# Kernel optimization log

Measured on AMD Instinct MI355X. Metric: run time of the kernel, lower is better.

## Reference

```python
import math
import jax, jax.numpy as jnp
import numpy as np

EPS = 1e-7
MAX_TANH_ARG = 1.0 - 1e-5

def _norm(x):
    return jnp.sqrt(jnp.sum(x * x, axis=-1, keepdims=True)).clip(EPS)

def logmap0(x):  # Poincare ball, c=1
    n = _norm(x)
    return jnp.arctanh(jnp.clip(n, EPS, MAX_TANH_ARG)) * x / n

def expmap0(v):
    n = _norm(v)
    return jnp.tanh(n) * v / n

def mobius_add(x, y):
    x2 = jnp.sum(x * x, -1, keepdims=True)
    y2 = jnp.sum(y * y, -1, keepdims=True)
    xy = jnp.sum(x * y, -1, keepdims=True)
    num = (1 + 2 * xy + y2) * x + (1 - x2) * y
    den = (1 + 2 * xy + x2 * y2).clip(EPS)
    return num / den

def plin(x, w, b):  # PoincareLinear: tangent-space affine map
    return expmap0(logmap0(x) @ w + b)

def layer_norm(x, eps=1e-6):  # elementwise_affine=False
    m = x.mean(-1, keepdims=True)
    v = ((x - m) ** 2).mean(-1, keepdims=True)
    return (x - m) / jnp.sqrt(v + eps)

def _beta(a, b):
    return math.exp(math.lgamma(a) + math.lgamma(b) - math.lgamma(a + b))

D, H, FF = 1024, 16, 4096
HD = D // H
BETA_N = _beta(D / 2, 0.5)   # beta(n/2, 1/2) for full dim
BETA_H = _beta(HD / 2, 0.5)  # beta(ni/2, 1/2) for head dim


def setup_inputs() -> dict:
    key = jax.random.key(0)
    ks = jax.random.split(key, 20)
    B, S = 4, 1024
    x = expmap0(0.02 * jax.random.normal(ks[0], (B, S, D), jnp.float32))
    t_emb = jax.random.normal(ks[1], (B, 1, D), jnp.float32)
    g = lambda k, sh: 0.02 * jax.random.normal(k, sh, jnp.float32)
    return {
        'x': x, 't_emb': t_emb,
        'w_q': g(ks[2], (D, D)), 'b_q': jnp.zeros((D,), jnp.float32),
        'w_k': g(ks[3], (D, D)), 'b_k': jnp.zeros((D,), jnp.float32),
        'w_v': g(ks[4], (D, D)), 'b_v': jnp.zeros((D,), jnp.float32),
        'w_o': g(ks[5], (D, D)), 'b_o': jnp.zeros((D,), jnp.float32),
        'w_f1': g(ks[6], (D, FF)), 'b_f1': jnp.zeros((FF,), jnp.float32),
        'w_f2': g(ks[7], (FF, D)), 'b_f2': jnp.zeros((D,), jnp.float32),
        'w_ada': g(ks[8], (D, 6 * D)), 'b_ada': jnp.zeros((6 * D,), jnp.float32),
    }


def _to_heads(p):
    # beta-split: logmap0, split per head, scale by beta_ni/beta_n, expmap0
    B, S, _ = p.shape
    t = logmap0(p).reshape(B, S, H, HD) * (BETA_H / BETA_N)
    return expmap0(jnp.transpose(t, (0, 2, 1, 3)))  # [B,H,S,HD]


def _from_heads(ph):
    # beta-concat: logmap0 per head, scale by beta_n/beta_ni, concat, expmap0
    B, _, S, _ = ph.shape
    t = logmap0(ph) * (BETA_N / BETA_H)
    t = jnp.transpose(t, (0, 2, 1, 3)).reshape(B, S, D)
    return expmap0(t)


def reference(x, t_emb, w_q, b_q, w_k, b_k, w_v, b_v, w_o, b_o,
              w_f1, b_f1, w_f2, b_f2, w_ada, b_ada):
    ada = t_emb @ w_ada + b_ada  # [B,1,6D]
    sh_msa, sc_msa, g_msa, sh_mlp, sc_mlp, g_mlp = jnp.split(ada, 6, axis=-1)

    # --- attention block ---
    residual = x
    xn = layer_norm(logmap0(x))
    xm = expmap0(xn * (1 + sc_msa) + sh_msa)

    q = _to_heads(plin(xm, w_q, b_q))
    k = _to_heads(plin(xm, w_k, b_k))
    v = _to_heads(plin(xm, w_v, b_v))

    qt, kt, vt = logmap0(q), logmap0(k), logmap0(v)
    scores = jnp.einsum('bhqd,bhkd->bhqk', qt, kt) / math.sqrt(HD)
    attn = jax.nn.softmax(scores, axis=-1)
    out_h = expmap0(jnp.einsum('bhqk,bhkd->bhqd', attn, vt))  # [B,H,S,HD]

    attn_out = plin(_from_heads(out_h), w_o, b_o)
    attn_t = g_msa * logmap0(attn_out)
    x = mobius_add(residual, expmap0(attn_t))

    # --- FFN block ---
    residual = x
    xn = layer_norm(logmap0(x))
    xm = expmap0(xn * (1 + sc_mlp) + sh_mlp)
    ff = plin(plin(xm, w_f1, b_f1), w_f2, b_f2)
    ff_t = g_mlp * logmap0(ff)
    return mobius_add(residual, expmap0(ff_t))
```

## Files before the change

### kernel.cpp

```cpp
#include <hip/hip_runtime.h>
#include <cmath>


constexpr int kD  = 1024;
constexpr int kH  = 16;
constexpr int kHD = 64;
constexpr int kFF = 4096;
constexpr int kB  = 4;
constexpr int kS  = 1024;
constexpr int kN  = kB * kS;

#define EPSF 1e-7f
#define MTAF (1.0f - 1e-5f)
#define LOG2E 1.4426950408889634f

typedef unsigned int uint32;
typedef unsigned short ushort16;
typedef __attribute__((ext_vector_type(8))) short short8x;
typedef __attribute__((ext_vector_type(4))) float floatx4;

__device__ __forceinline__ ushort16 f2b(float f) {
  union { float f; uint32 u; } x; x.f = f;
  uint32 r = x.u + 0x7fffu + ((x.u >> 16) & 1u);
  return (ushort16)(r >> 16);
}
__device__ __forceinline__ float b2f(ushort16 u) {
  union { uint32 u; float f; } x; x.u = ((uint32)u) << 16;
  return x.f;
}
__device__ __forceinline__ void load_b4(const ushort16* p, float v[4]) {
  uint2 u = *(const uint2*)p;
  v[0] = b2f((ushort16)(u.x & 0xffff)); v[1] = b2f((ushort16)(u.x >> 16));
  v[2] = b2f((ushort16)(u.y & 0xffff)); v[3] = b2f((ushort16)(u.y >> 16));
}
__device__ __forceinline__ void store_b4(ushort16* p, const float v[4]) {
  uint2 u;
  u.x = (uint32)f2b(v[0]) | ((uint32)f2b(v[1]) << 16);
  u.y = (uint32)f2b(v[2]) | ((uint32)f2b(v[3]) << 16);
  *(uint2*)p = u;
}

__device__ __forceinline__ float atanh_clipped(float n) {
  float c = fminf(n, MTAF);
  return 0.5f * logf((1.0f + c) / (1.0f - c));
}
__device__ __forceinline__ float logmap0_scale(float nraw) {
  float n = fmaxf(nraw, EPSF);
  return atanh_clipped(n) / n;
}
__device__ __forceinline__ float expmap0_scale(float nraw) {
  float n = fmaxf(nraw, EPSF);
  return tanhf(n) / n;
}
__device__ __forceinline__ float roundtrip_scale(float nraw) {
  float nu = fmaxf(nraw, EPSF);
  float se = tanhf(nu) / nu;
  float nb = fmaxf(se * nraw, EPSF);
  float sl = atanh_clipped(nb) / nb;
  return sl * se;
}

__device__ __forceinline__ float blockReduceSum256(float v, float* s4) {
#pragma unroll
  for (int o = 32; o > 0; o >>= 1) v += __shfl_xor(v, o);
  int wave = threadIdx.x >> 6;
  if ((threadIdx.x & 63) == 0) s4[wave] = v;
  __syncthreads();
  float r = s4[0] + s4[1] + s4[2] + s4[3];
  __syncthreads();
  return r;
}
__device__ __forceinline__ float redSum16(float v) {
#pragma unroll
  for (int o = 8; o > 0; o >>= 1) v += __shfl_xor(v, o);
  return v;
}

__device__ __forceinline__ void async16(const void* g, void* l) {
  __builtin_amdgcn_global_load_lds(
      (const __attribute__((address_space(1))) uint32*)g,
      (__attribute__((address_space(3))) uint32*)l, 16, 0, 0);
}

__device__ __forceinline__ void transpose_tile(const float* __restrict__ src,
                                               ushort16* __restrict__ dst,
                                               int K, int N, int n0, int k0) {
  __shared__ float T[64][65];
  int tid = threadIdx.x;
#pragma unroll
  for (int p = 0; p < 4; ++p) {
    int idx = p * 1024 + tid * 4;
    int r = idx >> 6, c = idx & 63;
    float4 t = *(const float4*)&src[(size_t)(k0 + r) * N + n0 + c];
    T[r][c] = t.x; T[r][c + 1] = t.y; T[r][c + 2] = t.z; T[r][c + 3] = t.w;
  }
  __syncthreads();
#pragma unroll
  for (int p = 0; p < 4; ++p) {
    int idx = p * 1024 + tid * 4;
    int r = idx >> 6, c = idx & 63;
    float v[4] = {T[c][r], T[c + 1][r], T[c + 2][r], T[c + 3][r]};
    store_b4(&dst[(size_t)(n0 + r) * K + k0 + c], v);
  }
}
__global__ __launch_bounds__(256) void k_transpose_bf16(const float* __restrict__ src,
                                                        ushort16* __restrict__ dst,
                                                        int K, int N) {
  transpose_tile(src, dst, K, N, blockIdx.x * 64, blockIdx.y * 64);
}
__global__ __launch_bounds__(256) void k_transpose4(
    const float* __restrict__ s0, const float* __restrict__ s1,
    const float* __restrict__ s2, const float* __restrict__ s3,
    ushort16* __restrict__ d0, ushort16* __restrict__ d1,
    ushort16* __restrict__ d2, ushort16* __restrict__ d3) {
  const float* src = (blockIdx.z == 0) ? s0 : (blockIdx.z == 1) ? s1
                    : (blockIdx.z == 2) ? s2 : s3;
  ushort16* dst = (blockIdx.z == 0) ? d0 : (blockIdx.z == 1) ? d1
                 : (blockIdx.z == 2) ? d2 : d3;
  transpose_tile(src, dst, kD, kD, blockIdx.x * 64, blockIdx.y * 64);
}

__global__ __launch_bounds__(256) void k_ada(const float* __restrict__ t_emb,
                                             const float* __restrict__ w_ada,
                                             const float* __restrict__ b_ada,
                                             float* __restrict__ ada) {
  __shared__ float te[kD];
  __shared__ float part[4][64];
  int b = blockIdx.y;
  int tid = threadIdx.x;
  {
    float4 t = *(const float4*)&t_emb[b * kD + tid * 4];
    te[tid * 4] = t.x; te[tid * 4 + 1] = t.y; te[tid * 4 + 2] = t.z; te[tid * 4 + 3] = t.w;
  }
  __syncthreads();
  int c = tid & 63, kc = tid >> 6;
  int col = blockIdx.x * 64 + c;
  float acc = 0.f;
#pragma unroll 8
  for (int k = kc * 256; k < kc * 256 + 256; ++k)
    acc += te[k] * w_ada[(size_t)k * (6 * kD) + col];
  part[kc][c] = acc;
  __syncthreads();
  if (tid < 64)
    ada[b * 6 * kD + blockIdx.x * 64 + tid] =
        part[0][tid] + part[1][tid] + part[2][tid] + part[3][tid] +
        b_ada[blockIdx.x * 64 + tid];
}

__global__ __launch_bounds__(256) void k_prenorm(const float* __restrict__ x,
                                                 const float* __restrict__ ada,
                                                 int sh_off, int sc_off,
                                                 ushort16* __restrict__ out) {
  __shared__ float sred[4];
  int tok = blockIdx.x;
  int b = tok >> 10;
  int d4 = threadIdx.x * 4;
  float xv[4];
  *(float4*)xv = *(const float4*)&x[(size_t)tok * kD + d4];
  float ss = xv[0] * xv[0] + xv[1] * xv[1] + xv[2] * xv[2] + xv[3] * xv[3];
  ss = blockReduceSum256(ss, sred);
  float sl = logmap0_scale(sqrtf(ss));
  float sum = 0.f;
#pragma unroll
  for (int i = 0; i < 4; ++i) { xv[i] *= sl; sum += xv[i]; }
  sum = blockReduceSum256(sum, sred);
  float mean = sum * (1.0f / kD);
  float vs = 0.f;
#pragma unroll
  for (int i = 0; i < 4; ++i) { xv[i] -= mean; vs += xv[i] * xv[i]; }
  vs = blockReduceSum256(vs, sred);
  float inv = rsqrtf(vs * (1.0f / kD) + 1e-6f);
  float shv[4], scv[4];
  *(float4*)shv = *(const float4*)&ada[b * 6 * kD + sh_off + d4];
  *(float4*)scv = *(const float4*)&ada[b * 6 * kD + sc_off + d4];
  float uu = 0.f;
#pragma unroll
  for (int i = 0; i < 4; ++i) {
    float u = xv[i] * inv * (1.0f + scv[i]) + shv[i];
    xv[i] = u;
    uu += u * u;
  }
  uu = blockReduceSum256(uu, sred);
  float s = roundtrip_scale(sqrtf(uu));
#pragma unroll
  for (int i = 0; i < 4; ++i) xv[i] *= s;
  store_b4(out + (size_t)tok * kD + d4, xv);
}

template <int OUT_BF16, int KSPLIT>
__global__ __launch_bounds__(256) void k_gemm_bf16(
    const ushort16* __restrict__ A,
    const ushort16* __restrict__ Bt0, const ushort16* __restrict__ Bt1,
    const ushort16* __restrict__ Bt2,
    const float* __restrict__ bias0, const float* __restrict__ bias1,
    const float* __restrict__ bias2,
    const float* __restrict__ rowscale,
    void* __restrict__ C0, void* __restrict__ C1, void* __restrict__ C2,
    int M, int N, int K) {
  const ushort16* Bt;
  const float* bias;
  void* C;
  int k_lo, k_hi;
  bool add_bias;
  if (KSPLIT == 1) {
    Bt = (blockIdx.z == 0) ? Bt0 : ((blockIdx.z == 1) ? Bt1 : Bt2);
    bias = (blockIdx.z == 0) ? bias0 : ((blockIdx.z == 1) ? bias1 : bias2);
    C = (blockIdx.z == 0) ? C0 : ((blockIdx.z == 1) ? C1 : C2);
    k_lo = 0; k_hi = K; add_bias = true;
  } else {
    Bt = Bt0; bias = bias0;
    C = (blockIdx.z == 0) ? C0 : C1;
    int kchunk = K / KSPLIT;
    k_lo = blockIdx.z * kchunk; k_hi = k_lo + kchunk;
    add_bias = (blockIdx.z == 0);
  }

  __shared__ __align__(16) ushort16 As[128 * 32];
  __shared__ __align__(16) ushort16 Bs[128 * 32];

  int tid = threadIdx.x;
  int lane = tid & 63;
  int wave = tid >> 6;
  int wm = (wave >> 1) * 64, wn = (wave & 1) * 64;
  int row0 = blockIdx.x * 128, col0 = blockIdx.y * 128;

  int e0 = tid * 8;
  int ar0 = e0 >> 5;
  int ac0 = ((((e0 >> 3) & 3) ^ ((ar0 >> 1) & 3)) << 3);
  int e1 = e0 + 2048;
  int ar1 = e1 >> 5;
  int ac1 = ((((e1 >> 3) & 3) ^ ((ar1 >> 1) & 3)) << 3);
  const ushort16* Ag = A + (size_t)row0 * K;
  const ushort16* Bg = Bt + (size_t)col0 * K;

  int c16 = lane & 15, quad = lane >> 4;
  int sw = (lane >> 1) & 3;
  int cbp = ((quad ^ sw) << 3);

  floatx4 acc[4][4];
#pragma unroll
  for (int i = 0; i < 4; ++i)
#pragma unroll
    for (int j = 0; j < 4; ++j) acc[i][j] = (floatx4)0.f;

  for (int k0 = k_lo; k0 < k_hi; k0 += 32) {
    async16(Ag + (size_t)ar0 * K + k0 + ac0, As + e0);
    async16(Ag + (size_t)ar1 * K + k0 + ac1, As + e1);
    async16(Bg + (size_t)ar0 * K + k0 + ac0, Bs + e0);
    async16(Bg + (size_t)ar1 * K + k0 + ac1, Bs + e1);
    __syncthreads();

    short8x a[4], b[4];
#pragma unroll
    for (int i = 0; i < 4; ++i) {
      a[i] = *(const short8x*)&As[(wm + i * 16 + c16) * 32 + cbp];
      b[i] = *(const short8x*)&Bs[(wn + i * 16 + c16) * 32 + cbp];
    }
#pragma unroll
    for (int i = 0; i < 4; ++i)
#pragma unroll
      for (int j = 0; j < 4; ++j)
        acc[i][j] = __builtin_amdgcn_mfma_f32_16x16x32_bf16(a[i], b[j], acc[i][j], 0, 0, 0);
    __syncthreads();
  }

  float bv[4];
#pragma unroll
  for (int j = 0; j < 4; ++j)
    bv[j] = add_bias ? bias[col0 + wn + j * 16 + c16] : 0.f;
  int rowq = quad * 4;
#pragma unroll
  for (int i = 0; i < 4; ++i) {
    int rbase = row0 + wm + i * 16 + rowq;
    float rs4[4];
#pragma unroll
    for (int r = 0; r < 4; ++r) rs4[r] = rowscale ? rowscale[rbase + r] : 1.0f;
#pragma unroll
    for (int j = 0; j < 4; ++j) {
      int c = col0 + wn + j * 16 + c16;
#pragma unroll
      for (int r = 0; r < 4; ++r) {
        float v = acc[i][j][r] * rs4[r] + bv[j];
        if (KSPLIT == 2) {
          if (blockIdx.z == 0) ((float*)C)[(size_t)(rbase + r) * N + c] = v;
          else ((ushort16*)C)[(size_t)(rbase + r) * N + c] = f2b(v);
        } else if (OUT_BF16) {
          ((ushort16*)C)[(size_t)(rbase + r) * N + c] = f2b(v);
        } else {
          ((float*)C)[(size_t)(rbase + r) * N + c] = v;
        }
      }
    }
  }
}

__global__ __launch_bounds__(256) void k_headsplit_b(const ushort16* __restrict__ q_in,
                                                     ushort16* __restrict__ k_io,
                                                     ushort16* __restrict__ v_io,
                                                     ushort16* __restrict__ qb_out,
                                                     float ratio) {
  __shared__ float sred[4];
  int tok = blockIdx.x;
  int tid = threadIdx.x;
  int d4 = tid * 4;
#pragma unroll
  for (int t = 0; t < 3; ++t) {
    const ushort16* p = (t == 0 ? q_in : (t == 1 ? (const ushort16*)k_io
                                                 : (const ushort16*)v_io)) +
                        (size_t)tok * kD + d4;
    float val[4];
    load_b4(p, val);
    float psq = val[0] * val[0] + val[1] * val[1] + val[2] * val[2] + val[3] * val[3];
    float hsq = redSum16(psq);
    float tot = blockReduceSum256(psq, sred);
    float s1 = roundtrip_scale(sqrtf(tot));
    float c = s1 * ratio;
    float s2 = roundtrip_scale(c * sqrtf(hsq));
    float f = c * s2 * (t == 0 ? (0.125f * LOG2E) : 1.0f);
#pragma unroll
    for (int i = 0; i < 4; ++i) val[i] *= f;
    ushort16* op = (t == 0 ? qb_out : (t == 1 ? k_io : v_io)) + (size_t)tok * kD + d4;
    store_b4(op, val);
    __syncthreads();
  }
}

__global__ __launch_bounds__(256) void k_vtrans_b(const ushort16* __restrict__ v,
                                                  ushort16* __restrict__ vT) {
  __shared__ ushort16 T[64][68];
  int bh = blockIdx.y, b = bh >> 4, h = bh & 15;
  int s0 = blockIdx.x * 64;
  int tid = threadIdx.x;
#pragma unroll
  for (int p = 0; p < 4; ++p) {
    int idx = p * 1024 + tid * 4;
    int r = idx >> 6, d = idx & 63;
    *(uint2*)&T[r][d] = *(const uint2*)&v[(size_t)(b * kS + s0 + r) * kD + h * kHD + d];
  }
  __syncthreads();
#pragma unroll
  for (int p = 0; p < 16; ++p) {
    int idx = p * 256 + tid;
    int d = idx >> 6, c = idx & 63;
    int cp = (c & 32) | ((c & 15) << 1) | ((c >> 4) & 1);
    vT[((size_t)bh * kHD + d) * kS + s0 + cp] = T[c][d];
  }
}

__global__ __launch_bounds__(256) void k_attn_mfma(ushort16* __restrict__ qb,
                                                   const ushort16* __restrict__ kb,
                                                   const ushort16* __restrict__ vT,
                                                   float ratio2) {
  __shared__ __align__(16) ushort16 Ks[2 * 128 * 32];
  __shared__ __align__(16) ushort16 Vs[4 * 64 * 32];
  __shared__ __align__(16) ushort16 Ps[4 * 4 * 16 * 40];
  int bh = blockIdx.x, b = bh >> 4, h = bh & 15;
  int q0 = blockIdx.y * 128;
  int tid = threadIdx.x, lane = tid & 63, wave = tid >> 6;
  int c16 = lane & 15, quad = lane >> 4;
  int sw = (lane >> 1) & 3;
  int cbp = ((quad ^ sw) << 3);
  int wq = wave * 32;

  short8x a_q[2][2];
#pragma unroll
  for (int i = 0; i < 2; ++i)
#pragma unroll
    for (int kk = 0; kk < 2; ++kk)
      a_q[i][kk] = *(const short8x*)&qb[(size_t)(b * kS + q0 + wq + i * 16 + c16) * kD +
                                        h * kHD + kk * 32 + quad * 8];

  short8x ones;
#pragma unroll
  for (int j = 0; j < 8; ++j) ones[j] = (short)0x3F80;

  floatx4 o[2][4], ol[2];
#pragma unroll
  for (int i = 0; i < 2; ++i) {
    ol[i] = (floatx4)0.f;
#pragma unroll
    for (int n = 0; n < 4; ++n) o[i][n] = (floatx4)0.f;
  }

  const ushort16* kbase = kb + ((size_t)b * kS) * kD + h * kHD;
  const ushort16* vbase = vT + (size_t)bh * kHD * kS;

  for (int k0 = 0; k0 < kS; k0 += 128) {
#pragma unroll
    for (int t = 0; t < 2; ++t)
#pragma unroll
      for (int cb2 = 0; cb2 < 2; ++cb2) {
        int e = cb2 * 2048 + tid * 8;
        int key = e >> 5;
        int col = ((((e >> 3) & 3) ^ ((key >> 1) & 3)) << 3);
        async16(kbase + (size_t)(k0 + key) * kD + t * 32 + col, Ks + t * 4096 + e);
      }
#pragma unroll
    for (int t = 0; t < 4; ++t) {
      int e = tid * 8;
      int dd = e >> 5;
      int col = ((((e >> 3) & 3) ^ ((dd >> 1) & 3)) << 3);
      async16(vbase + (size_t)dd * kS + k0 + t * 32 + col, Vs + t * 2048 + e);
    }
    __syncthreads();

#pragma unroll
    for (int i = 0; i < 2; ++i) {
      floatx4 s[8];
#pragma unroll
      for (int n = 0; n < 8; ++n) s[n] = (floatx4)0.f;
#pragma unroll
      for (int kkd = 0; kkd < 2; ++kkd)
#pragma unroll
        for (int n = 0; n < 8; ++n) {
          short8x bk = *(const short8x*)&Ks[kkd * 4096 + (n * 16 + c16) * 32 + cbp];
          s[n] = __builtin_amdgcn_mfma_f32_16x16x32_bf16(a_q[i][kkd], bk, s[n], 0, 0, 0);
        }

#pragma unroll
      for (int r = 0; r < 4; ++r) {
#pragma unroll
        for (int j = 0; j < 4; ++j) {
          uint32 u0 = (uint32)f2b(exp2f(s[2 * j][r]));
          uint32 u1 = (uint32)f2b(exp2f(s[2 * j + 1][r]));
          *(uint32*)&Ps[(((wave * 4 + j) * 16) + (quad * 4 + r)) * 40 + c16 * 2] =
              u0 | (u1 << 16);
        }
      }

#pragma unroll
      for (int kk = 0; kk < 4; ++kk) {
        short8x ap = *(const short8x*)&Ps[(((wave * 4 + kk) * 16) + c16) * 40 + quad * 8];
#pragma unroll
        for (int n = 0; n < 4; ++n) {
          short8x bv = *(const short8x*)&Vs[kk * 2048 + (n * 16 + c16) * 32 + cbp];
          o[i][n] = __builtin_amdgcn_mfma_f32_16x16x32_bf16(ap, bv, o[i][n], 0, 0, 0);
        }
        ol[i] = __builtin_amdgcn_mfma_f32_16x16x32_bf16(ap, ones, ol[i], 0, 0, 0);
      }
    }
    __syncthreads();
  }

#pragma unroll
  for (int i = 0; i < 2; ++i)
#pragma unroll
    for (int r = 0; r < 4; ++r) {
      float invl = 1.0f / ol[i][r];
      float w[4];
      float pssq = 0.f;
#pragma unroll
      for (int n = 0; n < 4; ++n) { w[n] = o[i][n][r] * invl; pssq += w[n] * w[n]; }
      float ssq = redSum16(pssq);
      float coef = roundtrip_scale(sqrtf(ssq)) * ratio2;
      int row = b * kS + q0 + wq + i * 16 + quad * 4 + r;
#pragma unroll
      for (int n = 0; n < 4; ++n)
        qb[(size_t)row * kD + h * kHD + n * 16 + c16] = f2b(coef * w[n]);
    }
}

template <int WIDTH>
__global__ __launch_bounds__(256) void k_rowscale(const ushort16* __restrict__ p,
                                                  float* __restrict__ s) {
  __shared__ float sred[4];
  constexpr int PER = WIDTH / 1024;
  size_t base = (size_t)blockIdx.x * WIDTH;
  float ss = 0.f;
#pragma unroll
  for (int i = 0; i < PER; ++i) {
    float v[4];
    load_b4(p + base + i * 1024 + threadIdx.x * 4, v);
    ss += v[0] * v[0] + v[1] * v[1] + v[2] * v[2] + v[3] * v[3];
  }
  ss = blockReduceSum256(ss, sred);
  if (threadIdx.x == 0) s[blockIdx.x] = roundtrip_scale(sqrtf(ss));
}

__device__ __forceinline__ void mobius_body(float xv[4], float tv[4],
                                            const float* gp, int d4,
                                            float* sred, float outv[4]) {
  float ss = tv[0] * tv[0] + tv[1] * tv[1] + tv[2] * tv[2] + tv[3] * tv[3];
  ss = blockReduceSum256(ss, sred);
  float s5 = roundtrip_scale(sqrtf(ss));
  float gv[4];
  *(float4*)gv = *(const float4*)&gp[d4];
  float at2 = 0.f;
#pragma unroll
  for (int i = 0; i < 4; ++i) {
    float a = gv[i] * s5 * tv[i];
    tv[i] = a;
    at2 += a * a;
  }
  at2 = blockReduceSum256(at2, sred);
  float nyraw = sqrtf(at2);
  float sy = expmap0_scale(nyraw);
  float ynorm = sy * nyraw;
  float y2 = ynorm * ynorm;
  float x2p = 0.f, xyp = 0.f;
#pragma unroll
  for (int i = 0; i < 4; ++i) {
    float y = sy * tv[i];
    tv[i] = y;
    x2p += xv[i] * xv[i];
    xyp += xv[i] * y;
  }
  float x2 = blockReduceSum256(x2p, sred);
  float xy = blockReduceSum256(xyp, sred);
  float cx = 1.0f + 2.0f * xy + y2;
  float cy = 1.0f - x2;
  float den = fmaxf(1.0f + 2.0f * xy + x2 * y2, EPSF);
  float invden = 1.0f / den;
#pragma unroll
  for (int i = 0; i < 4; ++i) outv[i] = (cx * xv[i] + cy * tv[i]) * invden;
}

__global__ __launch_bounds__(256) void k_epilogue2(const float* __restrict__ xres,
                                                   const float* __restrict__ ot0,
                                                   const ushort16* __restrict__ ot1b,
                                                   const float* __restrict__ ada,
                                                   int g_off,
                                                   float* __restrict__ out) {
  __shared__ float sred[4];
  int tok = blockIdx.x;
  int b = tok >> 10;
  size_t base = (size_t)tok * kD;
  int d4 = threadIdx.x * 4;
  float xv[4], tv[4], t1[4];
  *(float4*)tv = *(const float4*)&ot0[base + d4];
  load_b4(ot1b + base + d4, t1);
  *(float4*)xv = *(const float4*)&xres[base + d4];
#pragma unroll
  for (int i = 0; i < 4; ++i) tv[i] += t1[i];
  float outv[4];
  mobius_body(xv, tv, ada + b * 6 * kD + g_off, d4, sred, outv);
  *(float4*)&out[base + d4] = *(float4*)outv;
}

__global__ __launch_bounds__(256) void k_epi_pre(const float* __restrict__ xres,
                                                 const float* __restrict__ ot0,
                                                 const ushort16* __restrict__ ot1b,
                                                 const float* __restrict__ ada,
                                                 float* __restrict__ xmid_out,
                                                 ushort16* __restrict__ lx2_out) {
  __shared__ float sred[4];
  int tok = blockIdx.x;
  int b = tok >> 10;
  size_t base = (size_t)tok * kD;
  int d4 = threadIdx.x * 4;
  float xv[4], tv[4], t1[4];
  *(float4*)tv = *(const float4*)&ot0[base + d4];
  load_b4(ot1b + base + d4, t1);
  *(float4*)xv = *(const float4*)&xres[base + d4];
#pragma unroll
  for (int i = 0; i < 4; ++i) tv[i] += t1[i];
  float xm[4];
  mobius_body(xv, tv, ada + b * 6 * kD + 2 * kD, d4, sred, xm);
  *(float4*)&xmid_out[base + d4] = *(float4*)xm;

  float ss = xm[0] * xm[0] + xm[1] * xm[1] + xm[2] * xm[2] + xm[3] * xm[3];
  ss = blockReduceSum256(ss, sred);
  float sl = logmap0_scale(sqrtf(ss));
  float sum = 0.f;
#pragma unroll
  for (int i = 0; i < 4; ++i) { xm[i] *= sl; sum += xm[i]; }
  sum = blockReduceSum256(sum, sred);
  float mean = sum * (1.0f / kD);
  float vs = 0.f;
#pragma unroll
  for (int i = 0; i < 4; ++i) { xm[i] -= mean; vs += xm[i] * xm[i]; }
  vs = blockReduceSum256(vs, sred);
  float inv = rsqrtf(vs * (1.0f / kD) + 1e-6f);
  float shv[4], scv[4];
  *(float4*)shv = *(const float4*)&ada[b * 6 * kD + 3 * kD + d4];
  *(float4*)scv = *(const float4*)&ada[b * 6 * kD + 4 * kD + d4];
  float uu = 0.f;
#pragma unroll
  for (int i = 0; i < 4; ++i) {
    float u = xm[i] * inv * (1.0f + scv[i]) + shv[i];
    xm[i] = u;
    uu += u * u;
  }
  uu = blockReduceSum256(uu, sred);
  float s = roundtrip_scale(sqrtf(uu));
#pragma unroll
  for (int i = 0; i < 4; ++i) xm[i] *= s;
  store_b4(lx2_out + base + d4, xm);
}

extern "C" void kernel_launch(void* const* d_in, const int* in_sizes, int n_in,
                              void* d_out, int out_size, void* d_ws, size_t ws_size,
                              hipStream_t stream) {
  const float* x     = (const float*)d_in[0];
  const float* t_emb = (const float*)d_in[1];
  const float* w_q = (const float*)d_in[2];  const float* b_q = (const float*)d_in[3];
  const float* w_k = (const float*)d_in[4];  const float* b_k = (const float*)d_in[5];
  const float* w_v = (const float*)d_in[6];  const float* b_v = (const float*)d_in[7];
  const float* w_o = (const float*)d_in[8];  const float* b_o = (const float*)d_in[9];
  const float* w_f1 = (const float*)d_in[10]; const float* b_f1 = (const float*)d_in[11];
  const float* w_f2 = (const float*)d_in[12]; const float* b_f2 = (const float*)d_in[13];
  const float* w_ada = (const float*)d_in[14]; const float* b_ada = (const float*)d_in[15];
  float* out = (float*)d_out;

  constexpr size_t ND = (size_t)kN * kD;
  constexpr size_t NF = (size_t)kN * kFF;
  constexpr size_t DD = (size_t)kD * kD;

  float* ws   = (float*)d_ws;
  float* ada  = ws;
  float* qt   = ada + 6 * kD * kB;
  float* kt   = qt + ND;
  float* vt   = kt + ND;
  ushort16* qbA = (ushort16*)(vt + ND);
  ushort16* kb  = qbA + ND;
  ushort16* vTb = kb + ND;
  ushort16* actB = vTb + ND;
  ushort16* wqT  = actB + NF;
  ushort16* wkT  = wqT + DD;
  ushort16* wvT  = wkT + DD;
  ushort16* woT  = wvT + DD;
  ushort16* wf1T = woT + DD;
  ushort16* wf2T = wf1T + (size_t)kD * kFF;

  double bn = exp(lgamma(512.0) + lgamma(0.5) - lgamma(512.5));
  double bh = exp(lgamma(32.0) + lgamma(0.5) - lgamma(32.5));
  float R1 = (float)(bh / bn);
  float R2 = (float)(bn / bh);

  k_transpose4<<<dim3(16, 16, 4), 256, 0, stream>>>(w_q, w_k, w_v, w_o,
                                                    wqT, wkT, wvT, woT);
  k_transpose_bf16<<<dim3(64, 16), 256, 0, stream>>>(w_f1, wf1T, kD, kFF);
  k_transpose_bf16<<<dim3(16, 64), 256, 0, stream>>>(w_f2, wf2T, kFF, kD);
  k_ada<<<dim3(6 * kD / 64, kB), 256, 0, stream>>>(t_emb, w_ada, b_ada, ada);
  k_prenorm<<<kN, 256, 0, stream>>>(x, ada, 0 * kD, 1 * kD, qbA);
  k_gemm_bf16<1, 1><<<dim3(kN / 128, kD / 128, 3), 256, 0, stream>>>(
      qbA, wqT, wkT, wvT, b_q, b_k, b_v, nullptr, kb, vTb, actB, kN, kD, kD);
  k_headsplit_b<<<kN, 256, 0, stream>>>(kb, vTb, actB, qbA, R1);
  k_vtrans_b<<<dim3(kS / 64, kB * kH), 256, 0, stream>>>(actB, kb);
  k_attn_mfma<<<dim3(kB * kH, kS / 128), 256, 0, stream>>>(qbA, vTb, kb, R2);
  k_rowscale<kD><<<kN, 256, 0, stream>>>(qbA, kt);
  k_gemm_bf16<0, 2><<<dim3(kN / 128, kD / 128, 2), 256, 0, stream>>>(
      qbA, woT, woT, woT, b_o, b_o, b_o, kt, qt, kb, nullptr, kN, kD, kD);
  k_epi_pre<<<kN, 256, 0, stream>>>(x, qt, kb, ada, vt, qbA);
  k_gemm_bf16<1, 1><<<dim3(kN / 128, kFF / 128, 1), 256, 0, stream>>>(
      qbA, wf1T, wf1T, wf1T, b_f1, b_f1, b_f1, nullptr, actB, actB, actB, kN, kFF, kD);
  k_rowscale<kFF><<<kN, 256, 0, stream>>>(actB, kt);
  k_gemm_bf16<0, 2><<<dim3(kN / 128, kD / 128, 2), 256, 0, stream>>>(
      actB, wf2T, wf2T, wf2T, b_f2, b_f2, b_f2, kt, qt, kb, nullptr, kN, kD, kFF);
  k_epilogue2<<<kN, 256, 0, stream>>>(vt, qt, kb, ada, 5 * kD, out);

  (void)in_sizes; (void)n_in; (void)out_size; (void)ws_size;
}
```

Before: 452.2 us.

## Double-buffer GEMM with 256x128 tiles, BK=64, and async prefetch pipeline

Rewrites the bf16 GEMM to use 512-thread blocks over 256x128 output tiles with a K-step of 64. Shared memory is double-buffered, and the loads for step t+2 are issued while the MFMAs for step t run. The waits use explicit vmcnt/lgkmcnt counts and s_setprio around the MFMA bursts. The goal is to hide global-load latency and halve the barriers per K, at the cost of 96KB of LDS per block and a more fragile hand-counted wait scheme.

Result: faster. 432.5 us (-4.4%).

```diff
diff --git a/kernel.cpp b/kernel.cpp
--- a/kernel.cpp
+++ b/kernel.cpp
@@ -188,7 +188,7 @@
 }
 
 template <int OUT_BF16, int KSPLIT>
-__global__ __launch_bounds__(256) void k_gemm_bf16(
+__global__ __launch_bounds__(512, 2) void k_gemm_bf16(
     const ushort16* __restrict__ A,
     const ushort16* __restrict__ Bt0, const ushort16* __restrict__ Bt1,
     const ushort16* __restrict__ Bt2,
@@ -215,27 +215,39 @@
     add_bias = (blockIdx.z == 0);
   }
 
-  __shared__ __align__(16) ushort16 As[128 * 32];
-  __shared__ __align__(16) ushort16 Bs[128 * 32];
+  __shared__ __align__(16) ushort16 As[2 * 256 * 64];
+  __shared__ __align__(16) ushort16 Bs[2 * 128 * 64];
 
   int tid = threadIdx.x;
   int lane = tid & 63;
   int wave = tid >> 6;
-  int wm = (wave >> 1) * 64, wn = (wave & 1) * 64;
-  int row0 = blockIdx.x * 128, col0 = blockIdx.y * 128;
-
-  int e0 = tid * 8;
-  int ar0 = e0 >> 5;
-  int ac0 = ((((e0 >> 3) & 3) ^ ((ar0 >> 1) & 3)) << 3);
-  int e1 = e0 + 2048;
-  int ar1 = e1 >> 5;
-  int ac1 = ((((e1 >> 3) & 3) ^ ((ar1 >> 1) & 3)) << 3);
-  const ushort16* Ag = A + (size_t)row0 * K;
-  const ushort16* Bg = Bt + (size_t)col0 * K;
-
+  int wr = wave >> 1, wc = wave & 1;
   int c16 = lane & 15, quad = lane >> 4;
-  int sw = (lane >> 1) & 3;
-  int cbp = ((quad ^ sw) << 3);
+  int row0 = blockIdx.x * 256, col0 = blockIdx.y * 128;
+
+  int srow = tid >> 3;
+  int scol = (((tid & 7) ^ ((tid >> 4) & 7)) << 3);
+  const ushort16* a_src = A + (size_t)(row0 + srow) * K + k_lo + scol;
+  const ushort16* b_src = Bt + (size_t)(col0 + srow) * K + k_lo + scol;
+  int sdst = tid * 8;
+  int nt = (k_hi - k_lo) >> 6;
+
+  auto stage = [&](int tt) {
+    int cc = tt & 1;
+    size_t ko = (size_t)tt * 64;
+#pragma unroll
+    for (int p = 0; p < 4; ++p)
+      async16(a_src + ko + (size_t)(p * 64) * K, (ushort16*)As + cc * 16384 + p * 4096 + sdst);
+#pragma unroll
+    for (int p = 0; p < 2; ++p)
+      async16(b_src + ko + (size_t)(p * 64) * K, (ushort16*)Bs + cc * 8192 + p * 4096 + sdst);
+  };
+
+  int xsw = (c16 >> 1) & 7;
+  int aoff0 = (wr * 64 + c16) * 64 + ((quad ^ xsw) << 3);
+  int aoff1 = (wr * 64 + c16) * 64 + (((4 + quad) ^ xsw) << 3);
+  int boff0 = (wc * 64 + c16) * 64 + ((quad ^ xsw) << 3);
+  int boff1 = (wc * 64 + c16) * 64 + (((4 + quad) ^ xsw) << 3);
 
   floatx4 acc[4][4];
 #pragma unroll
@@ -243,41 +255,62 @@
 #pragma unroll
     for (int j = 0; j < 4; ++j) acc[i][j] = (floatx4)0.f;
 
-  for (int k0 = k_lo; k0 < k_hi; k0 += 32) {
-    async16(Ag + (size_t)ar0 * K + k0 + ac0, As + e0);
-    async16(Ag + (size_t)ar1 * K + k0 + ac1, As + e1);
-    async16(Bg + (size_t)ar0 * K + k0 + ac0, Bs + e0);
-    async16(Bg + (size_t)ar1 * K + k0 + ac1, Bs + e1);
-    __syncthreads();
-
-    short8x a[4], b[4];
+  stage(0);
+  stage(1);
+  asm volatile("s_waitcnt vmcnt(6)" ::: "memory");
+  __builtin_amdgcn_s_barrier();
+
+  for (int t = 0; t < nt; ++t) {
+    int cc = t & 1;
+    const ushort16* Ab = (const ushort16*)As + cc * 16384;
+    const ushort16* Bb = (const ushort16*)Bs + cc * 8192;
+    short8x a[4][2], b[4][2];
 #pragma unroll
     for (int i = 0; i < 4; ++i) {
-      a[i] = *(const short8x*)&As[(wm + i * 16 + c16) * 32 + cbp];
-      b[i] = *(const short8x*)&Bs[(wn + i * 16 + c16) * 32 + cbp];
+      a[i][0] = *(const short8x*)&Ab[i * 1024 + aoff0];
+      a[i][1] = *(const short8x*)&Ab[i * 1024 + aoff1];
+      b[i][0] = *(const short8x*)&Bb[i * 1024 + boff0];
+      b[i][1] = *(const short8x*)&Bb[i * 1024 + boff1];
     }
+    __builtin_amdgcn_s_setprio(1);
 #pragma unroll
     for (int i = 0; i < 4; ++i)
 #pragma unroll
       for (int j = 0; j < 4; ++j)
-        acc[i][j] = __builtin_amdgcn_mfma_f32_16x16x32_bf16(a[i], b[j], acc[i][j], 0, 0, 0);
-    __syncthreads();
+        acc[i][j] = __builtin_amdgcn_mfma_f32_16x16x32_bf16(a[i][0], b[j][0], acc[i][j], 0, 0, 0);
+    __builtin_amdgcn_s_setprio(0);
+    asm volatile("s_waitcnt lgkmcnt(0)" ::: "memory");
+    __builtin_amdgcn_s_barrier();
+    if (t + 2 < nt) stage(t + 2);
+    __builtin_amdgcn_s_setprio(1);
+#pragma unroll
+    for (int i = 0; i < 4; ++i)
+#pragma unroll
+      for (int j = 0; j < 4; ++j)
+        acc[i][j] = __builtin_amdgcn_mfma_f32_16x16x32_bf16(a[i][1], b[j][1], acc[i][j], 0, 0, 0);
+    __builtin_amdgcn_s_setprio(0);
+    if (t + 2 < nt) {
+      asm volatile("s_waitcnt vmcnt(6)" ::: "memory");
+    } else {
+      asm volatile("s_waitcnt vmcnt(0)" ::: "memory");
+    }
+    __builtin_amdgcn_s_barrier();
   }
 
   float bv[4];
 #pragma unroll
   for (int j = 0; j < 4; ++j)
-    bv[j] = add_bias ? bias[col0 + wn + j * 16 + c16] : 0.f;
+    bv[j] = add_bias ? bias[col0 + wc * 64 + j * 16 + c16] : 0.f;
   int rowq = quad * 4;
 #pragma unroll
   for (int i = 0; i < 4; ++i) {
-    int rbase = row0 + wm + i * 16 + rowq;
+    int rbase = row0 + wr * 64 + i * 16 + rowq;
     float rs4[4];
 #pragma unroll
     for (int r = 0; r < 4; ++r) rs4[r] = rowscale ? rowscale[rbase + r] : 1.0f;
 #pragma unroll
     for (int j = 0; j < 4; ++j) {
-      int c = col0 + wn + j * 16 + c16;
+      int c = col0 + wc * 64 + j * 16 + c16;
 #pragma unroll
       for (int r = 0; r < 4; ++r) {
         float v = acc[i][j][r] * rs4[r] + bv[j];
@@ -633,19 +666,19 @@
   k_transpose_bf16<<<dim3(16, 64), 256, 0, stream>>>(w_f2, wf2T, kFF, kD);
   k_ada<<<dim3(6 * kD / 64, kB), 256, 0, stream>>>(t_emb, w_ada, b_ada, ada);
   k_prenorm<<<kN, 256, 0, stream>>>(x, ada, 0 * kD, 1 * kD, qbA);
-  k_gemm_bf16<1, 1><<<dim3(kN / 128, kD / 128, 3), 256, 0, stream>>>(
+  k_gemm_bf16<1, 1><<<dim3(kN / 256, kD / 128, 3), 512, 0, stream>>>(
       qbA, wqT, wkT, wvT, b_q, b_k, b_v, nullptr, kb, vTb, actB, kN, kD, kD);
   k_headsplit_b<<<kN, 256, 0, stream>>>(kb, vTb, actB, qbA, R1);
   k_vtrans_b<<<dim3(kS / 64, kB * kH), 256, 0, stream>>>(actB, kb);
   k_attn_mfma<<<dim3(kB * kH, kS / 128), 256, 0, stream>>>(qbA, vTb, kb, R2);
   k_rowscale<kD><<<kN, 256, 0, stream>>>(qbA, kt);
-  k_gemm_bf16<0, 2><<<dim3(kN / 128, kD / 128, 2), 256, 0, stream>>>(
+  k_gemm_bf16<0, 2><<<dim3(kN / 256, kD / 128, 2), 512, 0, stream>>>(
       qbA, woT, woT, woT, b_o, b_o, b_o, kt, qt, kb, nullptr, kN, kD, kD);
   k_epi_pre<<<kN, 256, 0, stream>>>(x, qt, kb, ada, vt, qbA);
-  k_gemm_bf16<1, 1><<<dim3(kN / 128, kFF / 128, 1), 256, 0, stream>>>(
+  k_gemm_bf16<1, 1><<<dim3(kN / 256, kFF / 128, 1), 512, 0, stream>>>(
       qbA, wf1T, wf1T, wf1T, b_f1, b_f1, b_f1, nullptr, actB, actB, actB, kN, kFF, kD);
   k_rowscale<kFF><<<kN, 256, 0, stream>>>(actB, kt);
-  k_gemm_bf16<0, 2><<<dim3(kN / 128, kD / 128, 2), 256, 0, stream>>>(
+  k_gemm_bf16<0, 2><<<dim3(kN / 256, kD / 128, 2), 512, 0, stream>>>(
       actB, wf2T, wf2T, wf2T, b_f2, b_f2, b_f2, kt, qt, kb, nullptr, kN, kD, kFF);
   k_epilogue2<<<kN, 256, 0, stream>>>(vt, qt, kb, ada, 5 * kD, out);
 
```
